# Optimization experiments

Hardware: AMD Instinct MI355X
Metric: run time of the kernel (lower is better)

## Reference

```python
import jax, jax.numpy as jnp
import numpy as np

N_NODES = 50000


def gcn_conv(x, W, b, src, dst, n):
    # dense transform first (as PyG GCNConv does), then sparse aggregate
    h = x @ W  # [N, out]
    # add self loops
    loop = jnp.arange(n, dtype=src.dtype)
    s = jnp.concatenate([src, loop])
    d = jnp.concatenate([dst, loop])
    # symmetric normalization: deg over targets with unit edge weights
    deg = jax.ops.segment_sum(jnp.ones_like(d, dtype=h.dtype), d, num_segments=n)
    dinv = jnp.where(deg > 0, jax.lax.rsqrt(deg), 0.0)
    norm = dinv[s] * dinv[d]  # [E+N]
    msg = h[s] * norm[:, None]  # gather + scale
    out = jax.ops.segment_sum(msg, d, num_segments=n)  # scatter-add
    return out + b


def setup_inputs() -> dict:
    key = jax.random.key(0)
    k1, k2, k3, k4, k5 = jax.random.split(key, 5)
    in_dim, hid, out_dim = 256, 128, 16
    x = jax.random.normal(k1, (N_NODES, in_dim), dtype=jnp.float32)
    edge_index = jax.random.randint(k2, (2, 800000), 0, N_NODES, dtype=jnp.int64)
    # Glorot-style init for GCNConv weights, zero bias (PyG default)
    W1 = jax.random.normal(k3, (in_dim, hid), dtype=jnp.float32) / np.sqrt(in_dim)
    b1 = jnp.zeros((hid,), dtype=jnp.float32)
    W2 = jax.random.normal(k4, (hid, out_dim), dtype=jnp.float32) / np.sqrt(hid)
    b2 = jnp.zeros((out_dim,), dtype=jnp.float32)
    return {"x": x, "edge_index": edge_index, "W1": W1, "b1": b1, "W2": W2, "b2": b2}


def reference(x, edge_index, W1, b1, W2, b2):
    # eval-mode forward: dropout is identity
    src, dst = edge_index[0], edge_index[1]
    n = x.shape[0]
    h = gcn_conv(x, W1, b1, src, dst, n)
    h = jax.nn.relu(h)
    h = gcn_conv(h, W2, b2, src, dst, n)
    return jax.nn.log_softmax(h, axis=1)
```

## Files before the change

kernel.cpp:

```cpp
#include <hip/hip_runtime.h>
#include <hip/hip_bf16.h>

#define N_NODES 50000
#define E_EDGES 800000
#define IN_DIM  256
#define HID     128
#define OUT_DIM 16

#define NBUCK 391
#define NBLK  128
#define P2CAP 4096
#define GB1   391

using frag_ab = __attribute__((ext_vector_type(8))) short;
using frag_cd = __attribute__((ext_vector_type(4))) float;

static __device__ inline short f2bf(float f) {
    union { float f; unsigned u; } v; v.f = f;
    unsigned r = (v.u + 0x7fffu + ((v.u >> 16) & 1u)) >> 16;
    return (short)r;
}
static __device__ inline float bflo(unsigned u) {
    union { unsigned u; float f; } v; v.u = u << 16; return v.f;
}
static __device__ inline float bfhi(unsigned u) {
    union { unsigned u; float f; } v; v.u = u & 0xffff0000u; return v.f;
}
static __device__ inline unsigned packbf(float a, float b) {
    return (unsigned)(unsigned short)f2bf(a) | ((unsigned)(unsigned short)f2bf(b) << 16);
}

__global__ __launch_bounds__(512) void k1_gemm1_csra(const float* __restrict__ x,
                                                     const float* __restrict__ W1,
                                                     const int4* __restrict__ dst4,
                                                     const float* __restrict__ W2,
                                                     int* __restrict__ cnt_bb,
                                                     short* __restrict__ w2t,
                                                     short* __restrict__ h1s) {
    __shared__ uint4 lwt[64 * 64];
    int tid = threadIdx.x;

    if (blockIdx.x == GB1 + NBLK) {
        int n0 = tid >> 5, k0 = (tid & 31) * 4;
#pragma unroll
        for (int i = 0; i < 4; ++i)
            w2t[n0 * HID + k0 + i] = f2bf(W2[(k0 + i) * OUT_DIM + n0]);
        return;
    }
    if (blockIdx.x >= GB1) {
        int* hist = (int*)lwt;
        int bb = blockIdx.x - GB1;
        for (int i = tid; i < NBUCK; i += 512) hist[i] = 0;
        __syncthreads();
        for (int i = bb * 512 + tid; i < E_EDGES / 4; i += NBLK * 512) {
            int4 d = dst4[i];
            atomicAdd(&hist[d.x >> 7], 1);
            atomicAdd(&hist[d.y >> 7], 1);
            atomicAdd(&hist[d.z >> 7], 1);
            atomicAdd(&hist[d.w >> 7], 1);
        }
        __syncthreads();
        for (int i = tid; i < NBUCK; i += 512) cnt_bb[i * NBLK + bb] = hist[i];
        return;
    }

    {
        unsigned* lds32 = (unsigned*)lwt;
#pragma unroll
        for (int g = 0; g < 8; ++g) {
            int p = g * 512 + tid;
            int k = (p >> 5) * 2;
            int c4 = (p & 31) * 4;
            float4 A = *(const float4*)(W1 + (size_t)k * HID + c4);
            float4 B = *(const float4*)(W1 + (size_t)(k + 1) * HID + c4);
            int kt = k >> 5, q = (k >> 3) & 3, ip = (k >> 1) & 3;
            float av[4] = {A.x, A.y, A.z, A.w};
            float bv[4] = {B.x, B.y, B.z, B.w};
#pragma unroll
            for (int i = 0; i < 4; ++i) {
                int c = c4 + i;
                int tt = c >> 4, m = c & 15;
                lds32[4 * (((kt * 8 + tt) << 6) + (q << 4) + m) + ip] = packbf(av[i], bv[i]);
            }
        }
    }

    int wave = tid >> 6;
    int lane = tid & 63;
    int m = lane & 15;
    int q = lane >> 4;
    int row0 = blockIdx.x * 128 + wave * 16;
    int arow_idx = row0 + m;
    const float4* arow4 = (const float4*)(x + (size_t)(arow_idx < N_NODES ? arow_idx : 0) * IN_DIM);

    frag_ab a[8];
#pragma unroll
    for (int kt = 0; kt < 8; ++kt) {
        float4 f0 = arow4[kt * 8 + q * 2];
        float4 f1 = arow4[kt * 8 + q * 2 + 1];
        a[kt][0] = f2bf(f0.x); a[kt][1] = f2bf(f0.y); a[kt][2] = f2bf(f0.z); a[kt][3] = f2bf(f0.w);
        a[kt][4] = f2bf(f1.x); a[kt][5] = f2bf(f1.y); a[kt][6] = f2bf(f1.z); a[kt][7] = f2bf(f1.w);
    }

    frag_cd acc[8];
#pragma unroll
    for (int t = 0; t < 8; ++t) acc[t] = frag_cd{0.f, 0.f, 0.f, 0.f};

    __syncthreads();

#pragma unroll
    for (int kt = 0; kt < 8; ++kt) {
#pragma unroll
        for (int t = 0; t < 8; ++t) {
            frag_ab b = *(const frag_ab*)&lwt[(kt * 8 + t) * 64 + lane];
            acc[t] = __builtin_amdgcn_mfma_f32_16x16x32_bf16(a[kt], b, acc[t], 0, 0, 0);
        }
    }

#pragma unroll
    for (int t = 0; t < 8; ++t) {
#pragma unroll
        for (int r = 0; r < 4; ++r) {
            int orow = row0 + q * 4 + r;
            if (orow < N_NODES)
                h1s[(size_t)orow * HID + t * 16 + m] = f2bf(acc[t][r]);
        }
    }
}

__global__ __launch_bounds__(512) void csr_c2b(const int4* __restrict__ src4,
                                               const int4* __restrict__ dst4,
                                               const int* __restrict__ cnt_bb,
                                               int* __restrict__ bbase,
                                               unsigned* __restrict__ tmp) {
    __shared__ int run[NBUCK];
    __shared__ int sc[512];
    int t = threadIdx.x;
    int j = blockIdx.x;
    int tot = 0, pre = 0;
    if (t < NBUCK) {
        const int4* row = (const int4*)(cnt_bb + t * NBLK);
#pragma unroll 4
        for (int b4 = 0; b4 < NBLK / 4; ++b4) {
            int4 c = row[b4];
            int b = b4 * 4;
            tot += c.x + c.y + c.z + c.w;
            pre += (b + 0 < j ? c.x : 0) + (b + 1 < j ? c.y : 0)
                 + (b + 2 < j ? c.z : 0) + (b + 3 < j ? c.w : 0);
        }
    }
    sc[t] = tot;
    __syncthreads();
    for (int o = 1; o < 512; o <<= 1) {
        int u = (t >= o) ? sc[t - o] : 0;
        __syncthreads();
        sc[t] += u;
        __syncthreads();
    }
    if (t < NBUCK) {
        int exc = sc[t] - tot;
        run[t] = exc + pre;
        if (j == 0) bbase[t] = exc;
    }
    if (j == 0 && t == 511) bbase[NBUCK] = sc[511];
    __syncthreads();
    for (int i = j * 512 + t; i < E_EDGES / 4; i += NBLK * 512) {
        int4 d = dst4[i];
        int4 s = src4[i];
        int p0 = atomicAdd(&run[d.x >> 7], 1);
        tmp[p0] = (unsigned)s.x | ((unsigned)(d.x & 127) << 17);
        int p1 = atomicAdd(&run[d.y >> 7], 1);
        tmp[p1] = (unsigned)s.y | ((unsigned)(d.y & 127) << 17);
        int p2 = atomicAdd(&run[d.z >> 7], 1);
        tmp[p2] = (unsigned)s.z | ((unsigned)(d.z & 127) << 17);
        int p3 = atomicAdd(&run[d.w >> 7], 1);
        tmp[p3] = (unsigned)s.w | ((unsigned)(d.w & 127) << 17);
    }
}

__global__ __launch_bounds__(256) void csr_p2s(const unsigned* __restrict__ tmp,
                                               const int* __restrict__ bbase,
                                               int* __restrict__ rowptr,
                                               float* __restrict__ dinv,
                                               int* __restrict__ ssrc,
                                               short* __restrict__ h1s) {
    __shared__ unsigned ed[P2CAP];
    __shared__ int cnt[128];
    __shared__ int off[128];
    __shared__ float sdv[128];
    int b = blockIdx.x, t = threadIdx.x;
    int base = bbase[b];
    int m = bbase[b + 1] - base;
    if (m > P2CAP) m = P2CAP;
    if (t < 128) cnt[t] = 0;
    __syncthreads();
    for (int i = t; i < m; i += 256) {
        unsigned v = tmp[base + i];
        ed[i] = v;
        atomicAdd(&cnt[v >> 17], 1);
    }
    __syncthreads();
    if (t < 128) off[t] = cnt[t];
    __syncthreads();
    for (int o = 1; o < 128; o <<= 1) {
        int u = (t >= o && t < 128) ? off[t - o] : 0;
        __syncthreads();
        if (t < 128) off[t] += u;
        __syncthreads();
    }
    if (t < 128) {
        int node = b * 128 + t;
        int ex = off[t] - cnt[t];
        float dv = rsqrtf((float)(cnt[t] + 1));
        sdv[t] = dv;
        if (node < N_NODES) {
            rowptr[node] = base + ex;
            dinv[node] = dv;
        }
        off[t] = ex;
    }
    if (b == NBUCK - 1 && t == 0) rowptr[N_NODES] = E_EDGES;
    __syncthreads();
    for (int i = t; i < m; i += 256) {
        unsigned v = ed[i];
        int p = atomicAdd(&off[v >> 17], 1);
        ssrc[base + p] = (int)(v & 0x1FFFF);
    }
    for (int idx = t; idx < 128 * 16; idx += 256) {
        int nl = idx >> 4;
        int wd = idx & 15;
        int node = b * 128 + nl;
        if (node < N_NODES) {
            uint4* p = (uint4*)(h1s + (size_t)node * HID) + wd;
            uint4 u = *p;
            float dv = sdv[nl];
            u.x = packbf(dv * bflo(u.x), dv * bfhi(u.x));
            u.y = packbf(dv * bflo(u.y), dv * bfhi(u.y));
            u.z = packbf(dv * bflo(u.z), dv * bfhi(u.z));
            u.w = packbf(dv * bflo(u.w), dv * bfhi(u.w));
            *p = u;
        }
    }
}

__global__ __launch_bounds__(256) void agg1_pull(const short* __restrict__ h1s,
                                                 const float* __restrict__ dinv,
                                                 const float* __restrict__ b1,
                                                 const int* __restrict__ rowptr,
                                                 const int* __restrict__ ssrc,
                                                 uint4* __restrict__ out1) {
    int wave = threadIdx.x >> 6;
    int lane = threadIdx.x & 63;
    int node = __builtin_amdgcn_readfirstlane(blockIdx.x * 4 + wave);
    if (node >= N_NODES) return;
    int eo = lane >> 4;
    int g  = lane & 15;

    int lo = rowptr[node], hi = rowptr[node + 1];
    float dd = dinv[node];
    float a0 = 0.f, a1 = 0.f, a2 = 0.f, a3 = 0.f;
    float a4 = 0.f, a5 = 0.f, a6 = 0.f, a7 = 0.f;

    if (eo == 0) {
        uint4 u = *(const uint4*)(h1s + (size_t)node * HID + g * 8);
        a0 = bflo(u.x); a1 = bfhi(u.x); a2 = bflo(u.y); a3 = bfhi(u.y);
        a4 = bflo(u.z); a5 = bfhi(u.z); a6 = bflo(u.w); a7 = bfhi(u.w);
    }

    int e = lo;
    for (; e + 16 <= hi; e += 16) {
        int s0 = ssrc[e + eo];
        int s1 = ssrc[e + 4 + eo];
        int s2 = ssrc[e + 8 + eo];
        int s3 = ssrc[e + 12 + eo];
        uint4 u0 = *(const uint4*)(h1s + (size_t)s0 * HID + g * 8);
        uint4 u1 = *(const uint4*)(h1s + (size_t)s1 * HID + g * 8);
        uint4 u2 = *(const uint4*)(h1s + (size_t)s2 * HID + g * 8);
        uint4 u3 = *(const uint4*)(h1s + (size_t)s3 * HID + g * 8);
        a0 += bflo(u0.x); a1 += bfhi(u0.x); a2 += bflo(u0.y); a3 += bfhi(u0.y);
        a4 += bflo(u0.z); a5 += bfhi(u0.z); a6 += bflo(u0.w); a7 += bfhi(u0.w);
        a0 += bflo(u1.x); a1 += bfhi(u1.x); a2 += bflo(u1.y); a3 += bfhi(u1.y);
        a4 += bflo(u1.z); a5 += bfhi(u1.z); a6 += bflo(u1.w); a7 += bfhi(u1.w);
        a0 += bflo(u2.x); a1 += bfhi(u2.x); a2 += bflo(u2.y); a3 += bfhi(u2.y);
        a4 += bflo(u2.z); a5 += bfhi(u2.z); a6 += bflo(u2.w); a7 += bfhi(u2.w);
        a0 += bflo(u3.x); a1 += bfhi(u3.x); a2 += bflo(u3.y); a3 += bfhi(u3.y);
        a4 += bflo(u3.z); a5 += bfhi(u3.z); a6 += bflo(u3.w); a7 += bfhi(u3.w);
    }
    for (; e + 4 <= hi; e += 4) {
        int s = ssrc[e + eo];
        uint4 u = *(const uint4*)(h1s + (size_t)s * HID + g * 8);
        a0 += bflo(u.x); a1 += bfhi(u.x); a2 += bflo(u.y); a3 += bfhi(u.y);
        a4 += bflo(u.z); a5 += bfhi(u.z); a6 += bflo(u.w); a7 += bfhi(u.w);
    }
    if (eo < hi - e) {
        int s = ssrc[e + eo];
        uint4 u = *(const uint4*)(h1s + (size_t)s * HID + g * 8);
        a0 += bflo(u.x); a1 += bfhi(u.x); a2 += bflo(u.y); a3 += bfhi(u.y);
        a4 += bflo(u.z); a5 += bfhi(u.z); a6 += bflo(u.w); a7 += bfhi(u.w);
    }

    a0 += __shfl_xor(a0, 16); a1 += __shfl_xor(a1, 16);
    a2 += __shfl_xor(a2, 16); a3 += __shfl_xor(a3, 16);
    a4 += __shfl_xor(a4, 16); a5 += __shfl_xor(a5, 16);
    a6 += __shfl_xor(a6, 16); a7 += __shfl_xor(a7, 16);
    a0 += __shfl_xor(a0, 32); a1 += __shfl_xor(a1, 32);
    a2 += __shfl_xor(a2, 32); a3 += __shfl_xor(a3, 32);
    a4 += __shfl_xor(a4, 32); a5 += __shfl_xor(a5, 32);
    a6 += __shfl_xor(a6, 32); a7 += __shfl_xor(a7, 32);

    if (eo == 0) {
        float4 bA = *(const float4*)(b1 + g * 8);
        float4 bB = *(const float4*)(b1 + g * 8 + 4);
        float o0 = fmaxf(fmaf(dd, a0, bA.x), 0.f);
        float o1 = fmaxf(fmaf(dd, a1, bA.y), 0.f);
        float o2 = fmaxf(fmaf(dd, a2, bA.z), 0.f);
        float o3 = fmaxf(fmaf(dd, a3, bA.w), 0.f);
        float o4 = fmaxf(fmaf(dd, a4, bB.x), 0.f);
        float o5 = fmaxf(fmaf(dd, a5, bB.y), 0.f);
        float o6 = fmaxf(fmaf(dd, a6, bB.z), 0.f);
        float o7 = fmaxf(fmaf(dd, a7, bB.w), 0.f);
        uint4 st;
        st.x = packbf(o0, o1); st.y = packbf(o2, o3);
        st.z = packbf(o4, o5); st.w = packbf(o6, o7);
        out1[(size_t)node * 16 + g] = st;
    }
}

__global__ __launch_bounds__(256) void gemm2_mfma(const short* __restrict__ out1,
                                                  const short* __restrict__ w2t,
                                                  const float* __restrict__ dinv,
                                                  short* __restrict__ h2s) {
    int wave = threadIdx.x >> 6;
    int lane = threadIdx.x & 63;
    int m = lane & 15;
    int q = lane >> 4;
    int row0 = blockIdx.x * 64 + wave * 16;
    int arow = row0 + m;
    if (arow >= N_NODES) arow = N_NODES - 1;
    const short* ap = out1 + (size_t)arow * HID + q * 8;
    const short* bp = w2t + m * HID + q * 8;

    frag_cd acc = frag_cd{0.f, 0.f, 0.f, 0.f};
#pragma unroll
    for (int kt = 0; kt < 4; ++kt) {
        frag_ab a = *(const frag_ab*)(ap + kt * 32);
        frag_ab b = *(const frag_ab*)(bp + kt * 32);
        acc = __builtin_amdgcn_mfma_f32_16x16x32_bf16(a, b, acc, 0, 0, 0);
    }
#pragma unroll
    for (int r = 0; r < 4; ++r) {
        int row = row0 + q * 4 + r;
        if (row < N_NODES)
            h2s[(size_t)row * OUT_DIM + m] = f2bf(acc[r] * dinv[row]);
    }
}

__global__ __launch_bounds__(256) void agg2_pull(const unsigned* __restrict__ h2s,
                                                 const float* __restrict__ dinv,
                                                 const float* __restrict__ b2,
                                                 const int* __restrict__ rowptr,
                                                 const int* __restrict__ ssrc,
                                                 float* __restrict__ out) {
    int wave = threadIdx.x >> 6;
    int lane = threadIdx.x & 63;
    int node = __builtin_amdgcn_readfirstlane(blockIdx.x * 4 + wave);
    if (node >= N_NODES) return;
    int eo = lane >> 3;
    int g  = lane & 7;

    int lo = rowptr[node], hi = rowptr[node + 1];
    float a0 = 0.f, a1 = 0.f;
    if (eo == 0) {
        unsigned u = h2s[(size_t)node * 8 + g];
        a0 = bflo(u); a1 = bfhi(u);
    }
    int e = lo;
    for (; e + 16 <= hi; e += 16) {
        int s0 = ssrc[e + eo];
        int s1 = ssrc[e + 8 + eo];
        unsigned u0 = h2s[(size_t)s0 * 8 + g];
        unsigned u1 = h2s[(size_t)s1 * 8 + g];
        a0 += bflo(u0); a1 += bfhi(u0);
        a0 += bflo(u1); a1 += bfhi(u1);
    }
    for (; e + 8 <= hi; e += 8) {
        int s = ssrc[e + eo];
        unsigned u = h2s[(size_t)s * 8 + g];
        a0 += bflo(u); a1 += bfhi(u);
    }
    if (eo < hi - e) {
        int s = ssrc[e + eo];
        unsigned u = h2s[(size_t)s * 8 + g];
        a0 += bflo(u); a1 += bfhi(u);
    }

    a0 += __shfl_xor(a0, 8);  a1 += __shfl_xor(a1, 8);
    a0 += __shfl_xor(a0, 16); a1 += __shfl_xor(a1, 16);
    a0 += __shfl_xor(a0, 32); a1 += __shfl_xor(a1, 32);

    float dd = dinv[node];
    float2 bb = *(const float2*)(b2 + 2 * g);
    float v0 = fmaf(dd, a0, bb.x);
    float v1 = fmaf(dd, a1, bb.y);

    float m = fmaxf(v0, v1);
#pragma unroll
    for (int msk = 1; msk < 8; msk <<= 1) m = fmaxf(m, __shfl_xor(m, msk));
    float s2 = __expf(v0 - m) + __expf(v1 - m);
#pragma unroll
    for (int msk = 1; msk < 8; msk <<= 1) s2 += __shfl_xor(s2, msk);
    float lse = m + __logf(s2);
    if (eo == 0) {
        float2 o; o.x = v0 - lse; o.y = v1 - lse;
        *(float2*)(out + (size_t)node * OUT_DIM + 2 * g) = o;
    }
}

extern "C" void kernel_launch(void* const* d_in, const int* in_sizes, int n_in,
                              void* d_out, int out_size, void* d_ws, size_t ws_size,
                              hipStream_t stream) {
    const float* x  = (const float*)d_in[0];
    const int*   ei = (const int*)d_in[1];
    const float* W1 = (const float*)d_in[2];
    const float* b1 = (const float*)d_in[3];
    const float* W2 = (const float*)d_in[4];
    const float* b2 = (const float*)d_in[5];
    float* out = (float*)d_out;

    const int n = N_NODES;
    const int e = E_EDGES;
    const int* srcp = ei;
    const int* dstp = ei + e;

    char* w = (char*)d_ws;
    int*      cnt_bb = (int*)w;        w += (size_t)NBUCK * NBLK * 4;
    int*      bbase  = (int*)w;        w += (size_t)(NBUCK + 1) * 4;
    int*      rowptr = (int*)w;        w += (size_t)(n + 1) * 4;
    float*    dinv   = (float*)w;      w += (size_t)n * 4;
    unsigned* tmp    = (unsigned*)w;   w += (size_t)e * 4;
    int*      ssrc   = (int*)w;        w += (size_t)e * 4;
    short*    w2t    = (short*)w;      w += (size_t)OUT_DIM * HID * 2;
    short*    h1s    = (short*)w;      w += (size_t)n * HID * 2;
    short*    out1   = (short*)w;      w += (size_t)n * HID * 2;
    short*    h2s    = (short*)w;      w += (size_t)n * OUT_DIM * 2;

    auto blk = [](long long total, int b) { return (int)((total + b - 1) / b); };

    k1_gemm1_csra<<<GB1 + NBLK + 1, 512, 0, stream>>>(x, W1, (const int4*)dstp, W2,
                                                      cnt_bb, w2t, h1s);
    csr_c2b<<<NBLK, 512, 0, stream>>>((const int4*)srcp, (const int4*)dstp,
                                      cnt_bb, bbase, tmp);
    csr_p2s<<<NBUCK, 256, 0, stream>>>(tmp, bbase, rowptr, dinv, ssrc, h1s);
    agg1_pull<<<blk(n, 4), 256, 0, stream>>>(h1s, dinv, b1, rowptr, ssrc, (uint4*)out1);
    agg1_pull<<<blk(n, 4), 256, 0, stream>>>(h1s, dinv, b1, rowptr, ssrc, (uint4*)out1);
    gemm2_mfma<<<blk(n, 64), 256, 0, stream>>>(out1, w2t, dinv, h2s);
    agg2_pull<<<blk(n, 4), 256, 0, stream>>>((const unsigned*)h2s, dinv, b2,
                                             rowptr, ssrc, out);
}
```

Before: 230.1 us.

## Process two row tiles per GEMM1 block and drop duplicate agg1 launch

The first GEMM block now computes 256 rows instead of 128, reusing each LDS-staged W1 bf16 fragment for two MFMA accumulations. This halves the number of blocks that repack W1 into shared memory and lowers LDS traffic per output. A redundant second launch of agg1_pull, which recomputed identical results, is removed. The cost is a doubled register footprint for A fragments and accumulators, which may reduce occupancy.

Measured after the change: 193.2 us. 16.0% less time.

```diff
diff --git a/kernel.cpp b/kernel.cpp
--- a/kernel.cpp
+++ b/kernel.cpp
@@ -10,7 +10,7 @@
 #define NBUCK 391
 #define NBLK  128
 #define P2CAP 4096
-#define GB1   391
+#define GB1   196
 
 using frag_ab = __attribute__((ext_vector_type(8))) short;
 using frag_cd = __attribute__((ext_vector_type(4))) float;
@@ -89,22 +89,32 @@
     int lane = tid & 63;
     int m = lane & 15;
     int q = lane >> 4;
-    int row0 = blockIdx.x * 128 + wave * 16;
-    int arow_idx = row0 + m;
-    const float4* arow4 = (const float4*)(x + (size_t)(arow_idx < N_NODES ? arow_idx : 0) * IN_DIM);
-
-    frag_ab a[8];
+    int rowA0 = blockIdx.x * 256 + wave * 16;
+    int rowB0 = rowA0 + 128;
+    int arowA = rowA0 + m; if (arowA >= N_NODES) arowA = 0;
+    int arowB = rowB0 + m; if (arowB >= N_NODES) arowB = 0;
+    const float4* a4A = (const float4*)(x + (size_t)arowA * IN_DIM);
+    const float4* a4B = (const float4*)(x + (size_t)arowB * IN_DIM);
+
+    frag_ab aA[8], aB[8];
 #pragma unroll
     for (int kt = 0; kt < 8; ++kt) {
-        float4 f0 = arow4[kt * 8 + q * 2];
-        float4 f1 = arow4[kt * 8 + q * 2 + 1];
-        a[kt][0] = f2bf(f0.x); a[kt][1] = f2bf(f0.y); a[kt][2] = f2bf(f0.z); a[kt][3] = f2bf(f0.w);
-        a[kt][4] = f2bf(f1.x); a[kt][5] = f2bf(f1.y); a[kt][6] = f2bf(f1.z); a[kt][7] = f2bf(f1.w);
-    }
-
-    frag_cd acc[8];
-#pragma unroll
-    for (int t = 0; t < 8; ++t) acc[t] = frag_cd{0.f, 0.f, 0.f, 0.f};
+        float4 f0 = a4A[kt * 8 + q * 2];
+        float4 f1 = a4A[kt * 8 + q * 2 + 1];
+        aA[kt][0] = f2bf(f0.x); aA[kt][1] = f2bf(f0.y); aA[kt][2] = f2bf(f0.z); aA[kt][3] = f2bf(f0.w);
+        aA[kt][4] = f2bf(f1.x); aA[kt][5] = f2bf(f1.y); aA[kt][6] = f2bf(f1.z); aA[kt][7] = f2bf(f1.w);
+    }
+#pragma unroll
+    for (int kt = 0; kt < 8; ++kt) {
+        float4 f0 = a4B[kt * 8 + q * 2];
+        float4 f1 = a4B[kt * 8 + q * 2 + 1];
+        aB[kt][0] = f2bf(f0.x); aB[kt][1] = f2bf(f0.y); aB[kt][2] = f2bf(f0.z); aB[kt][3] = f2bf(f0.w);
+        aB[kt][4] = f2bf(f1.x); aB[kt][5] = f2bf(f1.y); aB[kt][6] = f2bf(f1.z); aB[kt][7] = f2bf(f1.w);
+    }
+
+    frag_cd accA[8], accB[8];
+#pragma unroll
+    for (int t = 0; t < 8; ++t) { accA[t] = frag_cd{0.f,0.f,0.f,0.f}; accB[t] = frag_cd{0.f,0.f,0.f,0.f}; }
 
     __syncthreads();
 
@@ -113,7 +123,8 @@
 #pragma unroll
         for (int t = 0; t < 8; ++t) {
             frag_ab b = *(const frag_ab*)&lwt[(kt * 8 + t) * 64 + lane];
-            acc[t] = __builtin_amdgcn_mfma_f32_16x16x32_bf16(a[kt], b, acc[t], 0, 0, 0);
+            accA[t] = __builtin_amdgcn_mfma_f32_16x16x32_bf16(aA[kt], b, accA[t], 0, 0, 0);
+            accB[t] = __builtin_amdgcn_mfma_f32_16x16x32_bf16(aB[kt], b, accB[t], 0, 0, 0);
         }
     }
 
@@ -121,9 +132,12 @@
     for (int t = 0; t < 8; ++t) {
 #pragma unroll
         for (int r = 0; r < 4; ++r) {
-            int orow = row0 + q * 4 + r;
-            if (orow < N_NODES)
-                h1s[(size_t)orow * HID + t * 16 + m] = f2bf(acc[t][r]);
+            int oA = rowA0 + q * 4 + r;
+            if (oA < N_NODES)
+                h1s[(size_t)oA * HID + t * 16 + m] = f2bf(accA[t][r]);
+            int oB = rowB0 + q * 4 + r;
+            if (oB < N_NODES)
+                h1s[(size_t)oB * HID + t * 16 + m] = f2bf(accB[t][r]);
         }
     }
 }
@@ -452,7 +466,6 @@
                                       cnt_bb, bbase, tmp);
     csr_p2s<<<NBUCK, 256, 0, stream>>>(tmp, bbase, rowptr, dinv, ssrc, h1s);
     agg1_pull<<<blk(n, 4), 256, 0, stream>>>(h1s, dinv, b1, rowptr, ssrc, (uint4*)out1);
-    agg1_pull<<<blk(n, 4), 256, 0, stream>>>(h1s, dinv, b1, rowptr, ssrc, (uint4*)out1);
     gemm2_mfma<<<blk(n, 64), 256, 0, stream>>>(out1, w2t, dinv, h2s);
     agg2_pull<<<blk(n, 4), 256, 0, stream>>>((const unsigned*)h2s, dinv, b2,
                                              rowptr, ssrc, out);
```
